# Kernel optimization log

Hardware: AMD Instinct MI355X
Metric: run time of the kernel (lower is better)

The kernel has to match this reference:

```python
import jax, jax.numpy as jnp
import numpy as np

B, L, C = 256, 196, 768      # batch, tokens (14x14 grid), token_dim
K = 2048                      # codebook size (num_tokens)
H = W = 14                    # h = int(sqrt(L)), w = L // h


def setup_inputs() -> dict:
    key = jax.random.key(0)
    k1, k2, k3 = jax.random.split(key, 3)
    in_feas = jax.random.normal(k1, (B, L, C), dtype=jnp.float32)
    codebook = jax.random.normal(k2, (K, C), dtype=jnp.float32)
    # Conv1d(in=C, out=1, kernel=3, padding=1, bias=False) weight: [1, C, 3]
    att_w = jax.random.normal(k3, (1, C, 3), dtype=jnp.float32) * 0.02
    return {"in_feas": in_feas, "codebook": codebook, "att_w": att_w}


def reference(in_feas, codebook, att_w):
    b, l, c = in_feas.shape
    flat = in_feas.reshape(-1, c)  # [B*L, C]

    # --- SOHO visual-dictionary (VQ) nearest-neighbour lookup ---
    d = (jnp.sum(flat * flat, axis=1, keepdims=True)
         - 2.0 * flat @ codebook.T
         + jnp.sum(codebook * codebook, axis=1)[None, :])  # [B*L, K]
    encoding_indices = jnp.argmin(d, axis=1)               # [B*L] int
    quantized = codebook[encoding_indices]                 # [B*L, C]
    # straight-through estimator: output = x + sg(q - x)
    vd_outputs = flat + jax.lax.stop_gradient(quantized - flat)

    idx_out = encoding_indices.reshape(-1, H, W)

    # --- attention branch (att=True, not_plus=False) ---
    # Conv1d(C->1, k=3, pad=1) applied to each token as a length-1 sequence:
    # only the center tap att_w[0, :, 1] multiplies real data (neighbors are
    # zero padding), so the conv reduces to a dot with the center weights.
    att = jax.nn.relu(vd_outputs @ att_w[0, :, 1])         # [B*L]
    att_mask = jax.nn.softmax(att.reshape(b, l, 1), axis=1)  # softmax over L

    vd_outputs = vd_outputs.reshape(b, l, c)
    out_feas = vd_outputs + in_feas * att_mask
    return out_feas, idx_out
```

## Files before the change

### kernel.cpp

```cpp
#include <hip/hip_runtime.h>

#define B_ 256
#define L_ 196
#define C_ 768
#define K_ 2048
#define BL_ 50176

typedef __attribute__((ext_vector_type(8))) short bf16x8;
typedef __attribute__((ext_vector_type(4))) float f32x4;

typedef const __attribute__((address_space(1))) void gas_void;
typedef __attribute__((address_space(3))) void las_void;

__device__ __forceinline__ unsigned short f2bf(float f) {
  unsigned u = __builtin_bit_cast(unsigned, f);
  u = u + 0x7FFFu + ((u >> 16) & 1u);
  return (unsigned short)(u >> 16);
}

__device__ __forceinline__ unsigned fmono(float f) {
  unsigned u = __builtin_bit_cast(unsigned, f);
  return u ^ ((unsigned)((int)u >> 31) | 0x80000000u);
}

__global__ __launch_bounds__(256) void precompute_kernel(
    const float* __restrict__ cb, const float* __restrict__ attw,
    unsigned short* __restrict__ cbb, double* __restrict__ norms64,
    float* __restrict__ norms32, float* __restrict__ ac) {
  int wave = threadIdx.x >> 6;
  int lane = threadIdx.x & 63;
  int k = blockIdx.x * 4 + wave;
  const float* row = cb + (size_t)k * C_;
  double n = 0.0, a = 0.0;
  for (int c = lane; c < C_; c += 64) {
    float v = row[c];
    cbb[(size_t)k * C_ + c] = f2bf(v);
    n = fma((double)v, (double)v, n);
    a = fma((double)v, (double)attw[c * 3 + 1], a);
  }
  for (int off = 32; off > 0; off >>= 1) {
    n += __shfl_down(n, off);
    a += __shfl_down(a, off);
  }
  if (lane == 0) {
    norms64[k] = n;
    norms32[k] = (float)n;
    ac[k] = (a > 0.0) ? (float)a : 0.0f;
  }
}

__global__ __launch_bounds__(256) void convert_kernel(
    const float* __restrict__ x, unsigned short* __restrict__ xb) {
  int i = blockIdx.x * 256 + threadIdx.x;
  float4 v = ((const float4*)x)[i];
  uint2 w;
  w.x = (unsigned)f2bf(v.x) | ((unsigned)f2bf(v.y) << 16);
  w.y = (unsigned)f2bf(v.z) | ((unsigned)f2bf(v.w) << 16);
  ((uint2*)xb)[i] = w;
}

__global__ __launch_bounds__(512, 2) void phase1_kernel(
    const unsigned short* __restrict__ xb,
    const unsigned short* __restrict__ cbb,
    const float* __restrict__ norms32, unsigned* __restrict__ ws_cand) {
  __shared__ unsigned short As[2][256 * 64];
  __shared__ unsigned short Bs[2][256 * 64];
  __shared__ float norms_s[256];
  __shared__ unsigned cands_s[256][12];

  int tid = threadIdx.x;
  int bid = blockIdx.x;
  int nblk = bid & 7;
  int mblk = bid >> 3;
  size_t row0 = (size_t)mblk * 256;
  int code0 = nblk * 256;

  int w = tid >> 6, l = tid & 63;
  int wm = w >> 2, wn = w & 3;
  int col16 = l & 15, quad = l >> 4;

  if (tid < 256) norms_s[tid] = norms32[code0 + tid];

  int crow = tid >> 3;
  int slotraw = (tid & 7) ^ (crow & 7);
  size_t off0 = (size_t)crow * C_ + (size_t)slotraw * 8;
  const unsigned short* abase = xb + row0 * C_ + off0;
  const unsigned short* bbase = cbb + (size_t)code0 * C_ + off0;
  char* alds = (char*)&As[0][0] + w * 1024;
  char* blds = (char*)&Bs[0][0] + w * 1024;

  auto stage = [&](int kt, int buf) {
    const unsigned short* a_ = abase + kt * 64;
    const unsigned short* b_ = bbase + kt * 64;
    char* al_ = alds + buf * 32768;
    char* bl_ = blds + buf * 32768;
#pragma unroll
    for (int i = 0; i < 4; ++i) {
      __builtin_amdgcn_global_load_lds((gas_void*)(a_ + (size_t)i * 64 * C_),
                                       (las_void*)(al_ + i * 8192), 16, 0, 0);
      __builtin_amdgcn_global_load_lds((gas_void*)(b_ + (size_t)i * 64 * C_),
                                       (las_void*)(bl_ + i * 8192), 16, 0, 0);
    }
  };

  f32x4 acc[8][4];
#pragma unroll
  for (int mt = 0; mt < 8; ++mt)
#pragma unroll
    for (int nt = 0; nt < 4; ++nt) acc[mt][nt] = (f32x4){0.f, 0.f, 0.f, 0.f};

  stage(0, 0);
  __syncthreads();

  for (int kt = 0; kt < 12; ++kt) {
    int buf = kt & 1;
    if (kt < 11) stage(kt + 1, buf ^ 1);
    const char* Ab = (const char*)&As[buf][0];
    const char* Bb = (const char*)&Bs[buf][0];
#pragma unroll
    for (int ks = 0; ks < 2; ++ks) {
      int sl = (ks * 4 + quad) ^ (col16 & 7);
      bf16x8 af[8], bf[4];
#pragma unroll
      for (int mt = 0; mt < 8; ++mt) {
        int row = wm * 128 + mt * 16 + col16;
        af[mt] = *(const bf16x8*)(Ab + row * 128 + sl * 16);
      }
#pragma unroll
      for (int nt = 0; nt < 4; ++nt) {
        int row = wn * 64 + nt * 16 + col16;
        bf[nt] = *(const bf16x8*)(Bb + row * 128 + sl * 16);
      }
#pragma unroll
      for (int mt = 0; mt < 8; ++mt)
#pragma unroll
        for (int nt = 0; nt < 4; ++nt)
          acc[mt][nt] = __builtin_amdgcn_mfma_f32_16x16x32_bf16(
              af[mt], bf[nt], acc[mt][nt], 0, 0, 0);
    }
    __syncthreads();
  }

#pragma unroll
  for (int mt = 0; mt < 8; ++mt) {
#pragma unroll
    for (int r = 0; r < 4; ++r) {
      unsigned keys[4];
#pragma unroll
      for (int nt = 0; nt < 4; ++nt) {
        int codel = wn * 64 + nt * 16 + col16;
        float d = fmaf(-2.0f, acc[mt][nt][r], norms_s[codel]);
        keys[nt] = (fmono(d) & 0xFFFFF800u) | (unsigned)(code0 + codel);
      }
      unsigned win[3];
#pragma unroll
      for (int rnd = 0; rnd < 3; ++rnd) {
        unsigned mn = min(min(keys[0], keys[1]), min(keys[2], keys[3]));
        mn = min(mn, (unsigned)__shfl_xor((int)mn, 1));
        mn = min(mn, (unsigned)__shfl_xor((int)mn, 2));
        mn = min(mn, (unsigned)__shfl_xor((int)mn, 4));
        mn = min(mn, (unsigned)__shfl_xor((int)mn, 8));
        win[rnd] = mn;
#pragma unroll
        for (int nt = 0; nt < 4; ++nt)
          if (keys[nt] == mn) keys[nt] = 0xFFFFFFFFu;
      }
      if (col16 == 0) {
        int t = wm * 128 + mt * 16 + quad * 4 + r;
        cands_s[t][wn * 3 + 0] = win[0];
        cands_s[t][wn * 3 + 1] = win[1];
        cands_s[t][wn * 3 + 2] = win[2];
      }
    }
  }
  __syncthreads();
  for (int i = tid; i < 256 * 12; i += 512) {
    int t = i / 12;
    int j = i - t * 12;
    ws_cand[(row0 + t) * 96 + nblk * 12 + j] = cands_s[t][j];
  }
}

__global__ __launch_bounds__(256) void phase2_kernel(
    const float* __restrict__ x, const float* __restrict__ cb,
    const unsigned* __restrict__ ws_cand, const double* __restrict__ norms64,
    int* __restrict__ out_idx) {
  __shared__ unsigned cl[32][100];
  __shared__ int rcode[32][6];
  __shared__ double rd[32][6];
  int tid = threadIdx.x;
  size_t tok0 = (size_t)blockIdx.x * 32;

  for (int i = tid; i < 32 * 96; i += 256) {
    int t = i / 96;
    int s = i - t * 96;
    cl[t][s] = ws_cand[tok0 * 96 + i];
  }
  __syncthreads();

  if (tid < 32) {
    unsigned best[6];
#pragma unroll
    for (int j = 0; j < 6; ++j) best[j] = 0xFFFFFFFFu;
    for (int s = 0; s < 96; ++s) {
      unsigned v = cl[tid][s];
      if (v < best[5]) {
        best[5] = v;
#pragma unroll
        for (int j = 5; j > 0; --j) {
          if (best[j] < best[j - 1]) {
            unsigned t = best[j];
            best[j] = best[j - 1];
            best[j - 1] = t;
          }
        }
      }
    }
#pragma unroll
    for (int j = 0; j < 6; ++j) rcode[tid][j] = (int)(best[j] & 0x7FFu);
  }
  __syncthreads();

  if (tid < 192) {
    int t = tid / 6;
    int j = tid - t * 6;
    int code = rcode[t][j];
    const float* xr = x + (tok0 + t) * (size_t)C_;
    const float* cr = cb + (size_t)code * C_;
    double s = 0.0;
    for (int c = 0; c < C_; c += 4) {
      float4 xa = *(const float4*)(xr + c);
      float4 ca = *(const float4*)(cr + c);
      s = fma((double)xa.x, (double)ca.x, s);
      s = fma((double)xa.y, (double)ca.y, s);
      s = fma((double)xa.z, (double)ca.z, s);
      s = fma((double)xa.w, (double)ca.w, s);
    }
    rd[t][j] = fma(-2.0, s, norms64[code]);
  }
  __syncthreads();

  if (tid < 32) {
    double bv = rd[tid][0];
    int bi = rcode[tid][0];
#pragma unroll
    for (int j = 1; j < 6; ++j) {
      double v = rd[tid][j];
      int i0 = rcode[tid][j];
      if (v < bv || (v == bv && i0 < bi)) {
        bv = v;
        bi = i0;
      }
    }
    out_idx[tok0 + tid] = bi;
  }
}

#define APAD 776
__global__ __launch_bounds__(256, 2) void argmin_fallback(
    const float* __restrict__ x, const float* __restrict__ cb,
    const unsigned short* __restrict__ cbb,
    const double* __restrict__ norms64, const float* __restrict__ norms32,
    int* __restrict__ out_idx) {
  __shared__ unsigned short Asf[32 * APAD];
  __shared__ float norms_s[K_];
  __shared__ unsigned int cands[32][48];
  __shared__ int rcode[32][6];
  __shared__ double rd[32][6];

  int tid = threadIdx.x;
  size_t tok0 = (size_t)blockIdx.x * 32;

  for (int i = tid; i < K_; i += 256) norms_s[i] = norms32[i];

  const float4* xin = (const float4*)(x + tok0 * C_);
  for (int i = tid; i < 32 * 192; i += 256) {
    int tok = i / 192;
    int c4 = i - tok * 192;
    float4 v = xin[i];
    uint2 w;
    w.x = (unsigned)f2bf(v.x) | ((unsigned)f2bf(v.y) << 16);
    w.y = (unsigned)f2bf(v.z) | ((unsigned)f2bf(v.w) << 16);
    *(uint2*)&Asf[tok * APAD + c4 * 4] = w;
  }
  __syncthreads();

  int wv = tid >> 6;
  int lane = tid & 63;
  int col = lane & 15;
  int quad = lane >> 4;

  const unsigned short* a0p = &Asf[(col)*APAD + quad * 8];
  const unsigned short* a1p = &Asf[(16 + col) * APAD + quad * 8];

  for (int chunk = 0; chunk < 4; ++chunk) {
    int code0 = chunk * 512 + wv * 128 + col;
    const unsigned short* bbase = cbb + (size_t)code0 * C_ + quad * 8;

    f32x4 acc[2][8];
#pragma unroll
    for (int m = 0; m < 2; ++m)
#pragma unroll
      for (int n = 0; n < 8; ++n) acc[m][n] = (f32x4){0.f, 0.f, 0.f, 0.f};

    bf16x8 ca0 = *(const bf16x8*)(a0p);
    bf16x8 ca1 = *(const bf16x8*)(a1p);
    bf16x8 cbf[8];
#pragma unroll
    for (int n = 0; n < 8; ++n)
      cbf[n] = *(const bf16x8*)(bbase + (size_t)n * 16 * C_);

    for (int ks = 0; ks < 24; ++ks) {
      bf16x8 na0, na1, nbf[8];
      if (ks < 23) {
        int k1 = (ks + 1) * 32;
        na0 = *(const bf16x8*)(a0p + k1);
        na1 = *(const bf16x8*)(a1p + k1);
#pragma unroll
        for (int n = 0; n < 8; ++n)
          nbf[n] = *(const bf16x8*)(bbase + (size_t)n * 16 * C_ + k1);
      }
#pragma unroll
      for (int n = 0; n < 8; ++n) {
        acc[0][n] = __builtin_amdgcn_mfma_f32_16x16x32_bf16(ca0, cbf[n],
                                                            acc[0][n], 0, 0, 0);
        acc[1][n] = __builtin_amdgcn_mfma_f32_16x16x32_bf16(ca1, cbf[n],
                                                            acc[1][n], 0, 0, 0);
      }
      if (ks < 23) {
        ca0 = na0;
        ca1 = na1;
#pragma unroll
        for (int n = 0; n < 8; ++n) cbf[n] = nbf[n];
      }
    }

#pragma unroll
    for (int m = 0; m < 2; ++m) {
#pragma unroll
      for (int r = 0; r < 4; ++r) {
        unsigned keys[8];
#pragma unroll
        for (int n = 0; n < 8; ++n) {
          int code = code0 + n * 16;
          float d = fmaf(-2.0f, acc[m][n][r], norms_s[code]);
          keys[n] = (fmono(d) & 0xFFFFF800u) | (unsigned)code;
        }
        unsigned win[3];
#pragma unroll
        for (int rnd = 0; rnd < 3; ++rnd) {
          unsigned mn = keys[0];
#pragma unroll
          for (int n = 1; n < 8; ++n) mn = min(mn, keys[n]);
          mn = min(mn, (unsigned)__shfl_xor((int)mn, 1));
          mn = min(mn, (unsigned)__shfl_xor((int)mn, 2));
          mn = min(mn, (unsigned)__shfl_xor((int)mn, 4));
          mn = min(mn, (unsigned)__shfl_xor((int)mn, 8));
          win[rnd] = mn;
#pragma unroll
          for (int n = 0; n < 8; ++n)
            if (keys[n] == mn) keys[n] = 0xFFFFFFFFu;
        }
        if (col == 0) {
          int token = m * 16 + quad * 4 + r;
          unsigned* cp = &cands[token][chunk * 12 + wv * 3];
          cp[0] = win[0];
          cp[1] = win[1];
          cp[2] = win[2];
        }
      }
    }
  }
  __syncthreads();

  if (tid < 32) {
    unsigned best[6];
#pragma unroll
    for (int j = 0; j < 6; ++j) best[j] = 0xFFFFFFFFu;
    for (int s = 0; s < 48; ++s) {
      unsigned v = cands[tid][s];
      if (v < best[5]) {
        best[5] = v;
#pragma unroll
        for (int j = 5; j > 0; --j) {
          if (best[j] < best[j - 1]) {
            unsigned t = best[j];
            best[j] = best[j - 1];
            best[j - 1] = t;
          }
        }
      }
    }
#pragma unroll
    for (int j = 0; j < 6; ++j) rcode[tid][j] = (int)(best[j] & 0x7FFu);
  }
  __syncthreads();

  if (tid < 192) {
    int t = tid / 6;
    int j = tid - t * 6;
    int code = rcode[t][j];
    const float* xr = x + (tok0 + t) * (size_t)C_;
    const float* cr = cb + (size_t)code * C_;
    double s = 0.0;
    for (int c = 0; c < C_; c += 4) {
      float4 xa = *(const float4*)(xr + c);
      float4 ca = *(const float4*)(cr + c);
      s = fma((double)xa.x, (double)ca.x, s);
      s = fma((double)xa.y, (double)ca.y, s);
      s = fma((double)xa.z, (double)ca.z, s);
      s = fma((double)xa.w, (double)ca.w, s);
    }
    rd[t][j] = fma(-2.0, s, norms64[code]);
  }
  __syncthreads();

  if (tid < 32) {
    double bv = rd[tid][0];
    int bi = rcode[tid][0];
#pragma unroll
    for (int j = 1; j < 6; ++j) {
      double v = rd[tid][j];
      int i0 = rcode[tid][j];
      if (v < bv || (v == bv && i0 < bi)) {
        bv = v;
        bi = i0;
      }
    }
    out_idx[tok0 + tid] = bi;
  }
}

__global__ __launch_bounds__(256) void epilogue_kernel(
    const float* __restrict__ x, const float* __restrict__ cb,
    const float* __restrict__ ac, const int* __restrict__ idx,
    float* __restrict__ out, float* __restrict__ out_idx) {
  __shared__ float att[256];
  __shared__ float red[256];
  __shared__ int ids[L_];
  int b = blockIdx.x;
  int tid = threadIdx.x;

  float a = -1e30f;
  int myid = 0;
  if (tid < L_) {
    myid = idx[b * L_ + tid];
    ids[tid] = myid;
    a = ac[myid];
  }
  att[tid] = a;
  red[tid] = a;
  __syncthreads();
  for (int s = 128; s > 0; s >>= 1) {
    if (tid < s) red[tid] = fmaxf(red[tid], red[tid + s]);
    __syncthreads();
  }
  float m = red[0];
  __syncthreads();
  float e = (tid < L_) ? expf(att[tid] - m) : 0.0f;
  red[tid] = e;
  __syncthreads();
  for (int s = 128; s > 0; s >>= 1) {
    if (tid < s) red[tid] += red[tid + s];
    __syncthreads();
  }
  float sum = red[0];
  __syncthreads();
  att[tid] = e / sum;
  __syncthreads();

  const float4* xin = (const float4*)(x + (size_t)b * L_ * C_);
  float4* o = (float4*)(out + (size_t)b * L_ * C_);
  for (int i = tid; i < L_ * (C_ / 4); i += 256) {
    int l = i / (C_ / 4);
    int c4 = i - l * (C_ / 4);
    const float4* crow = (const float4*)(cb + (size_t)ids[l] * C_);
    float4 xv = xin[i];
    float4 cv = crow[c4];
    float mk = att[l];
    float4 ov;
    ov.x = cv.x + xv.x * mk;
    ov.y = cv.y + xv.y * mk;
    ov.z = cv.z + xv.z * mk;
    ov.w = cv.w + xv.w * mk;
    o[i] = ov;
  }
  if (tid < L_) out_idx[b * L_ + tid] = (float)ids[tid];
}

extern "C" void kernel_launch(void* const* d_in, const int* in_sizes, int n_in,
                              void* d_out, int out_size, void* d_ws,
                              size_t ws_size, hipStream_t stream) {
  const float* in_feas = (const float*)d_in[0];
  const float* cb = (const float*)d_in[1];
  const float* attw = (const float*)d_in[2];

  char* ws = (char*)d_ws;
  size_t off = 0;
  unsigned short* cbb = (unsigned short*)(ws + off); off += 3145728;
  double* norms64 = (double*)(ws + off);           off += 16384;
  float* norms32 = (float*)(ws + off);             off += 8192;
  float* ac = (float*)(ws + off);                  off += 8192;
  int* idx = (int*)(ws + off);                     off += 200704;
  size_t base = off;
  unsigned short* xb = (unsigned short*)(ws + off); off += (size_t)BL_ * C_ * 2;
  unsigned* ws_cand = (unsigned*)(ws + off);        off += (size_t)BL_ * 96 * 4;
  size_t need_full = off;

  float* out = (float*)d_out;
  float* out_idx = out + (size_t)B_ * L_ * C_;

  precompute_kernel<<<K_ / 4, 256, 0, stream>>>(cb, attw, cbb, norms64,
                                                norms32, ac);
  if (ws_size >= need_full) {
    convert_kernel<<<BL_ * C_ / 4 / 256, 256, 0, stream>>>(in_feas, xb);
    phase1_kernel<<<dim3((BL_ / 256) * (K_ / 256)), 512, 0, stream>>>(
        xb, cbb, norms32, ws_cand);
    phase2_kernel<<<BL_ / 32, 256, 0, stream>>>(in_feas, cb, ws_cand, norms64,
                                                idx);
  } else {
    argmin_fallback<<<BL_ / 32, 256, 0, stream>>>(in_feas, cb, cbb, norms64,
                                                  norms32, idx);
  }
  epilogue_kernel<<<B_, 256, 0, stream>>>(in_feas, cb, ac, idx, out, out_idx);
  (void)base;
}
```

Before: 804.9 us.

## Pipeline phase1 GEMM in quadrant phases with block swizzle, widen epilogue blocks

Phase1 now splits the 256x256 tile into four 128x128 quadrant MFMA phases. Each phase is bracketed by barriers and s_setprio, with global-to-LDS staging for the next k-steps interleaved between phases and throttled by explicit vmcnt waits. Block indices are remapped so that groups of 8 blocks share codebook and row tiles, which should improve L2 reuse. The epilogue is relaunched with 1024 threads per block for more memory parallelism. The hand-written waitcnt schedule is fragile, and any mistake in it could cause data races.

New measurement: 796.4 us. No clear change (-1.1%).

```diff
diff --git a/kernel.cpp b/kernel.cpp
--- a/kernel.cpp
+++ b/kernel.cpp
@@ -63,113 +63,166 @@
     const unsigned short* __restrict__ xb,
     const unsigned short* __restrict__ cbb,
     const float* __restrict__ norms32, unsigned* __restrict__ ws_cand) {
-  __shared__ unsigned short As[2][256 * 64];
-  __shared__ unsigned short Bs[2][256 * 64];
+  __shared__ unsigned short lds[2][2][2][128 * 64];
   __shared__ float norms_s[256];
   __shared__ unsigned cands_s[256][12];
 
   int tid = threadIdx.x;
   int bid = blockIdx.x;
-  int nblk = bid & 7;
-  int mblk = bid >> 3;
+  int x8 = bid & 7, m = bid >> 3;
+  int mblk, nblk;
+  if (m < 192) {
+    mblk = (m & ~7) | x8;
+    nblk = m & 7;
+  } else {
+    mblk = m;
+    nblk = x8;
+  }
   size_t row0 = (size_t)mblk * 256;
   int code0 = nblk * 256;
 
-  int w = tid >> 6, l = tid & 63;
-  int wm = w >> 2, wn = w & 3;
+  int wv = tid >> 6, l = tid & 63;
+  int wm = wv >> 2, wn = wv & 3;
   int col16 = l & 15, quad = l >> 4;
 
   if (tid < 256) norms_s[tid] = norms32[code0 + tid];
 
-  int crow = tid >> 3;
-  int slotraw = (tid & 7) ^ (crow & 7);
-  size_t off0 = (size_t)crow * C_ + (size_t)slotraw * 8;
-  const unsigned short* abase = xb + row0 * C_ + off0;
-  const unsigned short* bbase = cbb + (size_t)code0 * C_ + off0;
-  char* alds = (char*)&As[0][0] + w * 1024;
-  char* blds = (char*)&Bs[0][0] + w * 1024;
-
-  auto stage = [&](int kt, int buf) {
-    const unsigned short* a_ = abase + kt * 64;
-    const unsigned short* b_ = bbase + kt * 64;
-    char* al_ = alds + buf * 32768;
-    char* bl_ = blds + buf * 32768;
-#pragma unroll
-    for (int i = 0; i < 4; ++i) {
-      __builtin_amdgcn_global_load_lds((gas_void*)(a_ + (size_t)i * 64 * C_),
-                                       (las_void*)(al_ + i * 8192), 16, 0, 0);
-      __builtin_amdgcn_global_load_lds((gas_void*)(b_ + (size_t)i * 64 * C_),
-                                       (las_void*)(bl_ + i * 8192), 16, 0, 0);
-    }
+  int slotraw = (tid & 7) ^ ((tid >> 3) & 7);
+  const unsigned short* abase = xb + (row0 + (tid >> 3)) * (size_t)C_ +
+                                (size_t)slotraw * 8;
+  const unsigned short* bbase = cbb + ((size_t)code0 + (tid >> 3)) * C_ +
+                                (size_t)slotraw * 8;
+
+  auto stageA = [&](int kt, int half, int buf) {
+    const unsigned short* s =
+        abase + (size_t)half * 128 * C_ + (size_t)kt * 64;
+    char* d = (char*)&lds[buf][0][half][0] + wv * 1024;
+    __builtin_amdgcn_global_load_lds((gas_void*)s, (las_void*)d, 16, 0, 0);
+    __builtin_amdgcn_global_load_lds((gas_void*)(s + (size_t)64 * C_),
+                                     (las_void*)(d + 8192), 16, 0, 0);
   };
-
-  f32x4 acc[8][4];
-#pragma unroll
-  for (int mt = 0; mt < 8; ++mt)
-#pragma unroll
-    for (int nt = 0; nt < 4; ++nt) acc[mt][nt] = (f32x4){0.f, 0.f, 0.f, 0.f};
-
-  stage(0, 0);
-  __syncthreads();
+  auto stageB = [&](int kt, int half, int buf) {
+    const unsigned short* s =
+        bbase + (size_t)half * 128 * C_ + (size_t)kt * 64;
+    char* d = (char*)&lds[buf][1][half][0] + wv * 1024;
+    __builtin_amdgcn_global_load_lds((gas_void*)s, (las_void*)d, 16, 0, 0);
+    __builtin_amdgcn_global_load_lds((gas_void*)(s + (size_t)64 * C_),
+                                     (las_void*)(d + 8192), 16, 0, 0);
+  };
+
+  f32x4 acc[2][2][4][2];
+#pragma unroll
+  for (int mh = 0; mh < 2; ++mh)
+#pragma unroll
+    for (int nh = 0; nh < 2; ++nh)
+#pragma unroll
+      for (int mt = 0; mt < 4; ++mt)
+#pragma unroll
+        for (int nt = 0; nt < 2; ++nt)
+          acc[mh][nh][mt][nt] = (f32x4){0.f, 0.f, 0.f, 0.f};
+
+  bf16x8 af[4][2], bfr[2][2];
+
+#define LOADA(P)                                                            \
+  _Pragma("unroll") for (int mt = 0; mt < 4; ++mt)                          \
+      _Pragma("unroll") for (int ks = 0; ks < 2; ++ks) af[mt][ks] =         \
+      *(const bf16x8*)((P) + (wm * 64 + mt * 16 + col16) * 128 +            \
+                       (((ks * 4 + quad) ^ (col16 & 7)) * 16));
+
+#define LOADB(P)                                                            \
+  _Pragma("unroll") for (int nt = 0; nt < 2; ++nt)                          \
+      _Pragma("unroll") for (int ks = 0; ks < 2; ++ks) bfr[nt][ks] =        \
+      *(const bf16x8*)((P) + (wn * 32 + nt * 16 + col16) * 128 +            \
+                       (((ks * 4 + quad) ^ (col16 & 7)) * 16));
+
+#define MFMA_PHASE(mh, nh)                                                  \
+  __builtin_amdgcn_s_barrier();                                             \
+  asm volatile("s_waitcnt lgkmcnt(0)" ::: "memory");                        \
+  __builtin_amdgcn_s_setprio(1);                                            \
+  _Pragma("unroll") for (int mt = 0; mt < 4; ++mt)                          \
+      _Pragma("unroll") for (int nt = 0; nt < 2; ++nt)                      \
+          _Pragma("unroll") for (int ks = 0; ks < 2; ++ks) acc[mh][nh][mt]  \
+      [nt] = __builtin_amdgcn_mfma_f32_16x16x32_bf16(                       \
+          af[mt][ks], bfr[nt][ks], acc[mh][nh][mt][nt], 0, 0, 0);           \
+  __builtin_amdgcn_s_setprio(0);                                            \
+  __builtin_amdgcn_s_barrier();
+
+  stageA(0, 0, 0);
+  stageB(0, 1, 0);
+  stageA(0, 1, 0);
+  stageB(0, 0, 0);
+  stageA(1, 0, 1);
+  stageB(1, 1, 1);
+  stageA(1, 1, 1);
+  asm volatile("s_waitcnt vmcnt(6)" ::: "memory");
+  __builtin_amdgcn_s_barrier();
 
   for (int kt = 0; kt < 12; ++kt) {
     int buf = kt & 1;
-    if (kt < 11) stage(kt + 1, buf ^ 1);
-    const char* Ab = (const char*)&As[buf][0];
-    const char* Bb = (const char*)&Bs[buf][0];
-#pragma unroll
-    for (int ks = 0; ks < 2; ++ks) {
-      int sl = (ks * 4 + quad) ^ (col16 & 7);
-      bf16x8 af[8], bf[4];
-#pragma unroll
-      for (int mt = 0; mt < 8; ++mt) {
-        int row = wm * 128 + mt * 16 + col16;
-        af[mt] = *(const bf16x8*)(Ab + row * 128 + sl * 16);
-      }
-#pragma unroll
-      for (int nt = 0; nt < 4; ++nt) {
-        int row = wn * 64 + nt * 16 + col16;
-        bf[nt] = *(const bf16x8*)(Bb + row * 128 + sl * 16);
-      }
-#pragma unroll
-      for (int mt = 0; mt < 8; ++mt)
-#pragma unroll
-        for (int nt = 0; nt < 4; ++nt)
-          acc[mt][nt] = __builtin_amdgcn_mfma_f32_16x16x32_bf16(
-              af[mt], bf[nt], acc[mt][nt], 0, 0, 0);
-    }
-    __syncthreads();
-  }
-
-#pragma unroll
-  for (int mt = 0; mt < 8; ++mt) {
-#pragma unroll
-    for (int r = 0; r < 4; ++r) {
-      unsigned keys[4];
-#pragma unroll
-      for (int nt = 0; nt < 4; ++nt) {
-        int codel = wn * 64 + nt * 16 + col16;
-        float d = fmaf(-2.0f, acc[mt][nt][r], norms_s[codel]);
-        keys[nt] = (fmono(d) & 0xFFFFF800u) | (unsigned)(code0 + codel);
-      }
-      unsigned win[3];
-#pragma unroll
-      for (int rnd = 0; rnd < 3; ++rnd) {
-        unsigned mn = min(min(keys[0], keys[1]), min(keys[2], keys[3]));
-        mn = min(mn, (unsigned)__shfl_xor((int)mn, 1));
-        mn = min(mn, (unsigned)__shfl_xor((int)mn, 2));
-        mn = min(mn, (unsigned)__shfl_xor((int)mn, 4));
-        mn = min(mn, (unsigned)__shfl_xor((int)mn, 8));
-        win[rnd] = mn;
-#pragma unroll
-        for (int nt = 0; nt < 4; ++nt)
-          if (keys[nt] == mn) keys[nt] = 0xFFFFFFFFu;
-      }
-      if (col16 == 0) {
-        int t = wm * 128 + mt * 16 + quad * 4 + r;
-        cands_s[t][wn * 3 + 0] = win[0];
-        cands_s[t][wn * 3 + 1] = win[1];
-        cands_s[t][wn * 3 + 2] = win[2];
+    const char* A0p = (const char*)&lds[buf][0][0][0];
+    const char* A1p = (const char*)&lds[buf][0][1][0];
+    const char* B0p = (const char*)&lds[buf][1][0][0];
+    const char* B1p = (const char*)&lds[buf][1][1][0];
+
+    if (kt + 1 < 12) stageB(kt + 1, 0, buf ^ 1);
+    LOADA(A0p);
+    LOADB(B0p);
+    MFMA_PHASE(0, 0);
+    if (kt + 2 < 12) stageA(kt + 2, 0, buf);
+    LOADB(B1p);
+    MFMA_PHASE(0, 1);
+    if (kt + 2 < 12) stageB(kt + 2, 1, buf);
+    LOADA(A1p);
+    MFMA_PHASE(1, 1);
+    if (kt + 2 < 12) stageA(kt + 2, 1, buf);
+    if (kt <= 9) {
+      asm volatile("s_waitcnt vmcnt(6)" ::: "memory");
+    } else if (kt == 10) {
+      asm volatile("s_waitcnt vmcnt(0)" ::: "memory");
+    }
+    LOADB(B0p);
+    MFMA_PHASE(1, 0);
+  }
+
+#undef LOADA
+#undef LOADB
+#undef MFMA_PHASE
+
+#pragma unroll
+  for (int mh = 0; mh < 2; ++mh) {
+#pragma unroll
+    for (int mt = 0; mt < 4; ++mt) {
+#pragma unroll
+      for (int r = 0; r < 4; ++r) {
+        unsigned keys[4];
+#pragma unroll
+        for (int nh = 0; nh < 2; ++nh)
+#pragma unroll
+          for (int nt = 0; nt < 2; ++nt) {
+            int codel = nh * 128 + wn * 32 + nt * 16 + col16;
+            float d = fmaf(-2.0f, acc[mh][nh][mt][nt][r], norms_s[codel]);
+            keys[nh * 2 + nt] =
+                (fmono(d) & 0xFFFFF800u) | (unsigned)(code0 + codel);
+          }
+        unsigned win[3];
+#pragma unroll
+        for (int rnd = 0; rnd < 3; ++rnd) {
+          unsigned mn = min(min(keys[0], keys[1]), min(keys[2], keys[3]));
+          mn = min(mn, (unsigned)__shfl_xor((int)mn, 1));
+          mn = min(mn, (unsigned)__shfl_xor((int)mn, 2));
+          mn = min(mn, (unsigned)__shfl_xor((int)mn, 4));
+          mn = min(mn, (unsigned)__shfl_xor((int)mn, 8));
+          win[rnd] = mn;
+#pragma unroll
+          for (int nt = 0; nt < 4; ++nt)
+            if (keys[nt] == mn) keys[nt] = 0xFFFFFFFFu;
+        }
+        if (col16 == 0) {
+          int t = mh * 128 + wm * 64 + mt * 16 + quad * 4 + r;
+          cands_s[t][wn * 3 + 0] = win[0];
+          cands_s[t][wn * 3 + 1] = win[1];
+          cands_s[t][wn * 3 + 2] = win[2];
+        }
       }
     }
   }
@@ -431,7 +484,7 @@
   }
 }
 
-__global__ __launch_bounds__(256) void epilogue_kernel(
+__global__ __launch_bounds__(1024) void epilogue_kernel(
     const float* __restrict__ x, const float* __restrict__ cb,
     const float* __restrict__ ac, const int* __restrict__ idx,
     float* __restrict__ out, float* __restrict__ out_idx) {
@@ -441,24 +494,28 @@
   int b = blockIdx.x;
   int tid = threadIdx.x;
 
-  float a = -1e30f;
-  int myid = 0;
-  if (tid < L_) {
-    myid = idx[b * L_ + tid];
-    ids[tid] = myid;
-    a = ac[myid];
-  }
-  att[tid] = a;
-  red[tid] = a;
+  float e = 0.0f;
+  if (tid < 256) {
+    float a = -1e30f;
+    if (tid < L_) {
+      int myid = idx[b * L_ + tid];
+      ids[tid] = myid;
+      a = ac[myid];
+    }
+    att[tid] = a;
+    red[tid] = a;
+  }
   __syncthreads();
   for (int s = 128; s > 0; s >>= 1) {
     if (tid < s) red[tid] = fmaxf(red[tid], red[tid + s]);
     __syncthreads();
   }
-  float m = red[0];
-  __syncthreads();
-  float e = (tid < L_) ? expf(att[tid] - m) : 0.0f;
-  red[tid] = e;
+  float mx = red[0];
+  __syncthreads();
+  if (tid < 256) {
+    e = (tid < L_) ? expf(att[tid] - mx) : 0.0f;
+    red[tid] = e;
+  }
   __syncthreads();
   for (int s = 128; s > 0; s >>= 1) {
     if (tid < s) red[tid] += red[tid + s];
@@ -466,12 +523,12 @@
   }
   float sum = red[0];
   __syncthreads();
-  att[tid] = e / sum;
+  if (tid < 256) att[tid] = e / sum;
   __syncthreads();
 
   const float4* xin = (const float4*)(x + (size_t)b * L_ * C_);
   float4* o = (float4*)(out + (size_t)b * L_ * C_);
-  for (int i = tid; i < L_ * (C_ / 4); i += 256) {
+  for (int i = tid; i < L_ * (C_ / 4); i += 1024) {
     int l = i / (C_ / 4);
     int c4 = i - l * (C_ / 4);
     const float4* crow = (const float4*)(cb + (size_t)ids[l] * C_);
@@ -522,6 +579,6 @@
     argmin_fallback<<<BL_ / 32, 256, 0, stream>>>(in_feas, cb, cbb, norms64,
                                                   norms32, idx);
   }
-  epilogue_kernel<<<B_, 256, 0, stream>>>(in_feas, cb, ac, idx, out, out_idx);
+  epilogue_kernel<<<B_, 1024, 0, stream>>>(in_feas, cb, ac, idx, out, out_idx);
   (void)base;
 }
```
